# Kernel optimization log

Measured on AMD Instinct MI355X. Metric: run time of the kernel, lower is better.

The kernel has to match this reference:

```python
import jax, jax.numpy as jnp
import numpy as np

MAX_LENGTH = 256
WIDTH = 4


def _attention_matrix(a, b):
    # a, b: (B, M, D) with M = max_length + width - 1
    # euclidean match score: 1 / (1 + ||a_i - b_j||_2)
    sq = (
        jnp.sum(a * a, axis=-1)[:, :, None]
        + jnp.sum(b * b, axis=-1)[:, None, :]
        - 2.0 * jnp.einsum('bid,bjd->bij', a, b)
    )
    dist = jnp.sqrt(jnp.maximum(sq, 0.0))
    return 1.0 / (1.0 + dist)  # (B, M, M)


def reference(x1, x2):
    # x1, x2: (B, 1, M, D), M = MAX_LENGTH + WIDTH - 1
    a = x1[:, 0]  # (B, M, D)
    b = x2[:, 0]
    A = _attention_matrix(a, b)  # (B, M, M), A[b,i,j] = score(a_i, b_j)
    # row_sum over dim i of A[:,:,k] weights x1 column k; col analogously for x2.
    w_a = jnp.sum(A, axis=1)  # (B, M): sum_i A[i, k]
    w_b = jnp.sum(A, axis=2)  # (B, M): sum_j A[k, j]
    y1 = w_a[:, :, None] * a  # (B, M, D)
    y2 = w_b[:, :, None] * b
    # sliding-window sum of width WIDTH: w[j] = sum_{k=j}^{j+WIDTH-1} y[k]
    w1 = sum(y1[:, d:d + MAX_LENGTH, :] for d in range(WIDTH))
    w2 = sum(y2[:, d:d + MAX_LENGTH, :] for d in range(WIDTH))
    return (w1[:, None], w2[:, None])  # (B, 1, MAX_LENGTH, D) each


def setup_inputs() -> dict:
    key = jax.random.key(0)
    k1, k2 = jax.random.split(key)
    B, M, D = 128, MAX_LENGTH + WIDTH - 1, 512
    x1 = jax.random.normal(k1, (B, 1, M, D), dtype=jnp.float32)
    x2 = jax.random.normal(k2, (B, 1, M, D), dtype=jnp.float32)
    return {"x1": x1, "x2": x2}
```

## Files before the change

kernel.cpp:

```cpp
#include <hip/hip_runtime.h>

#define BATCH 128
#define M 259
#define D 512
#define T 256
#define NM (BATCH * M)
#define OUTHALF (BATCH * T * D)

typedef __bf16 bf16;
typedef __bf16 bf16x4 __attribute__((ext_vector_type(4)));
typedef __bf16 bf16x8 __attribute__((ext_vector_type(8)));
typedef float f32x4 __attribute__((ext_vector_type(4)));


__global__ void k_norms(const float* __restrict__ x1, const float* __restrict__ x2,
                        float* __restrict__ ws) {
    int row  = blockIdx.x * 4 + (threadIdx.x >> 6);
    int lane = threadIdx.x & 63;
    if (row >= NM) return;
    const float4* p1 = (const float4*)(x1 + (size_t)row * D);
    const float4* p2 = (const float4*)(x2 + (size_t)row * D);
    float s1 = 0.f, s2 = 0.f;
#pragma unroll
    for (int q = 0; q < 2; ++q) {
        float4 v = p1[lane + q * 64];
        s1 += v.x * v.x + v.y * v.y + v.z * v.z + v.w * v.w;
        float4 u = p2[lane + q * 64];
        s2 += u.x * u.x + u.y * u.y + u.z * u.z + u.w * u.w;
    }
#pragma unroll
    for (int off = 32; off > 0; off >>= 1) {
        s1 += __shfl_xor(s1, off);
        s2 += __shfl_xor(s2, off);
    }
    if (lane == 0) {
        ws[row]          = s1;
        ws[NM + row]     = s2;
        ws[2 * NM + row] = 0.f;
        ws[3 * NM + row] = 0.f;
    }
}

#define BT 144
#define BK 64

__global__ void k_pairs(const float* __restrict__ x1, const float* __restrict__ x2,
                        float* __restrict__ ws) {
    __shared__ __align__(16) bf16 As[BT * BK];
    __shared__ __align__(16) bf16 Bs[BT * BK];

    int s   = blockIdx.x;
    int bid = (s & 7) * 64 + (s >> 3);
    int b   = bid >> 2;
    int ti  = (bid >> 1) & 1;
    int tj  = bid & 1;
    int i0  = ti * BT, j0 = tj * BT;

    int t    = threadIdx.x;
    int lane = t & 63;
    int w    = t / 64;
    int wm   = w / 3, wn = w % 3;
    int iw   = i0 + wm * 48;
    int jw   = j0 + wn * 48;

    const float* Ab = x1 + (size_t)b * M * D;
    const float* Bb = x2 + (size_t)b * M * D;

    const float* pa[4];
    const float* pb[4];
    int c4 = (t & 15) * 4;
#pragma unroll
    for (int p = 0; p < 4; ++p) {
        int row = p * 36 + (t >> 4);
        int ra = min(i0 + row, M - 1);
        int rb = min(j0 + row, M - 1);
        pa[p] = Ab + (size_t)ra * D + c4;
        pb[p] = Bb + (size_t)rb * D + c4;
    }
    int wslot   = (t & 15) >> 1;
    int wwithin = (t & 1) * 4;
    int wr_off[4];
#pragma unroll
    for (int p = 0; p < 4; ++p) {
        int row = p * 36 + (t >> 4);
        wr_off[p] = row * BK + ((wslot ^ (row & 7)) << 3) + wwithin;
    }

    int a_off[3][2], b_off[3][2];
#pragma unroll
    for (int fm = 0; fm < 3; ++fm) {
        int rowa = wm * 48 + fm * 16 + (lane & 15);
        int rowb = wn * 48 + fm * 16 + (lane & 15);
#pragma unroll
        for (int kk = 0; kk < 2; ++kk) {
            int slot = kk * 4 + (lane >> 4);
            a_off[fm][kk] = rowa * BK + ((slot ^ (rowa & 7)) << 3);
            b_off[fm][kk] = rowb * BK + ((slot ^ (rowb & 7)) << 3);
        }
    }

    f32x4 acc[3][3];
#pragma unroll
    for (int fm = 0; fm < 3; ++fm)
#pragma unroll
        for (int fn = 0; fn < 3; ++fn) acc[fm][fn] = (f32x4)0.f;

    for (int k0 = 0; k0 < D; k0 += BK) {
        float4 va[4], vb[4];
#pragma unroll
        for (int p = 0; p < 4; ++p) {
            va[p] = *(const float4*)(pa[p] + k0);
            vb[p] = *(const float4*)(pb[p] + k0);
        }
        __syncthreads();
#pragma unroll
        for (int p = 0; p < 4; ++p) {
            *(bf16x4*)&As[wr_off[p]] = bf16x4{ (bf16)va[p].x, (bf16)va[p].y, (bf16)va[p].z, (bf16)va[p].w };
            *(bf16x4*)&Bs[wr_off[p]] = bf16x4{ (bf16)vb[p].x, (bf16)vb[p].y, (bf16)vb[p].z, (bf16)vb[p].w };
        }
        __syncthreads();
#pragma unroll
        for (int kk = 0; kk < 2; ++kk) {
            bf16x8 af[3], bfr[3];
#pragma unroll
            for (int fm = 0; fm < 3; ++fm) af[fm]  = *(const bf16x8*)&As[a_off[fm][kk]];
#pragma unroll
            for (int fn = 0; fn < 3; ++fn) bfr[fn] = *(const bf16x8*)&Bs[b_off[fn][kk]];
#pragma unroll
            for (int fm = 0; fm < 3; ++fm)
#pragma unroll
                for (int fn = 0; fn < 3; ++fn)
                    acc[fm][fn] = __builtin_amdgcn_mfma_f32_16x16x32_bf16(
                        af[fm], bfr[fn], acc[fm][fn], 0, 0, 0);
        }
    }

    int b_off_w = b * M;
    float na_[3][4], nb_[3];
#pragma unroll
    for (int fm = 0; fm < 3; ++fm)
#pragma unroll
        for (int r = 0; r < 4; ++r) {
            int i = iw + fm * 16 + (lane >> 4) * 4 + r;
            na_[fm][r] = (i < M) ? ws[b_off_w + i] : 0.f;
        }
#pragma unroll
    for (int fn = 0; fn < 3; ++fn) {
        int j = jw + fn * 16 + (lane & 15);
        nb_[fn] = (j < M) ? ws[NM + b_off_w + j] : 0.f;
    }

    float rs[3][4], cs[3];
#pragma unroll
    for (int fm = 0; fm < 3; ++fm)
#pragma unroll
        for (int r = 0; r < 4; ++r) rs[fm][r] = 0.f;
#pragma unroll
    for (int fn = 0; fn < 3; ++fn) cs[fn] = 0.f;

#pragma unroll
    for (int fm = 0; fm < 3; ++fm) {
#pragma unroll
        for (int fn = 0; fn < 3; ++fn) {
#pragma unroll
            for (int r = 0; r < 4; ++r) {
                int i = iw + fm * 16 + (lane >> 4) * 4 + r;
                int j = jw + fn * 16 + (lane & 15);
                float av = 0.f;
                if (i < M && j < M) {
                    float sq   = na_[fm][r] + nb_[fn] - 2.f * acc[fm][fn][r];
                    float dist = sqrtf(fmaxf(sq, 0.f));
                    av = 1.f / (1.f + dist);
                }
                rs[fm][r] += av;
                cs[fn]    += av;
            }
        }
    }

#pragma unroll
    for (int fm = 0; fm < 3; ++fm)
#pragma unroll
        for (int r = 0; r < 4; ++r) {
            float v = rs[fm][r];
            v += __shfl_xor(v, 1); v += __shfl_xor(v, 2);
            v += __shfl_xor(v, 4); v += __shfl_xor(v, 8);
            int i = iw + fm * 16 + (lane >> 4) * 4 + r;
            if ((lane & 15) == 0 && i < M) atomicAdd(&ws[3 * NM + b_off_w + i], v);
        }
#pragma unroll
    for (int fn = 0; fn < 3; ++fn) {
        float v = cs[fn];
        v += __shfl_xor(v, 16); v += __shfl_xor(v, 32);
        int j = jw + fn * 16 + (lane & 15);
        if ((lane >> 4) == 0 && j < M) atomicAdd(&ws[2 * NM + b_off_w + j], v);
    }
}

__global__ void k_out(const float* __restrict__ x1, const float* __restrict__ x2,
                      const float* __restrict__ ws, float* __restrict__ out) {
    int bid   = blockIdx.x;
    int which = bid & 1;
    int tc    = (bid >> 1) & 7;
    int b     = bid >> 4;
    int d4    = threadIdx.x << 2;
    const float* src  = which ? x2 : x1;
    const float* wgt  = ws + (which ? 3 * NM : 2 * NM) + b * M;
    const float* rows = src + (size_t)b * M * D + d4;
    float* o = out + (size_t)which * OUTHALF + ((size_t)b * T + tc * 32) * D + d4;
    int t0 = tc * 32;
    float4 v0 = *(const float4*)(rows + (size_t)(t0 + 0) * D);
    float4 v1 = *(const float4*)(rows + (size_t)(t0 + 1) * D);
    float4 v2 = *(const float4*)(rows + (size_t)(t0 + 2) * D);
    float s0 = wgt[t0 + 0], s1 = wgt[t0 + 1], s2 = wgt[t0 + 2];
#pragma unroll 4
    for (int tt = 0; tt < 32; ++tt) {
        float4 v3 = *(const float4*)(rows + (size_t)(t0 + tt + 3) * D);
        float s3  = wgt[t0 + tt + 3];
        float4 r;
        r.x = s0 * v0.x + s1 * v1.x + s2 * v2.x + s3 * v3.x;
        r.y = s0 * v0.y + s1 * v1.y + s2 * v2.y + s3 * v3.y;
        r.z = s0 * v0.z + s1 * v1.z + s2 * v2.z + s3 * v3.z;
        r.w = s0 * v0.w + s1 * v1.w + s2 * v2.w + s3 * v3.w;
        *(float4*)(o + (size_t)tt * D) = r;
        v0 = v1; v1 = v2; v2 = v3;
        s0 = s1; s1 = s2; s2 = s3;
    }
}

extern "C" void kernel_launch(void* const* d_in, const int* in_sizes, int n_in,
                              void* d_out, int out_size, void* d_ws, size_t ws_size,
                              hipStream_t stream) {
    const float* x1 = (const float*)d_in[0];
    const float* x2 = (const float*)d_in[1];
    float* out = (float*)d_out;
    float* ws  = (float*)d_ws;

    k_norms<<<NM / 4, 256, 0, stream>>>(x1, x2, ws);
    k_pairs<<<512, 576, 0, stream>>>(x1, x2, ws);
    k_out<<<BATCH * 16, 128, 0, stream>>>(x1, x2, ws, out);
}
```

Baseline: 119.3 us.

## Replace shared-memory 144x144 tiles with single-wave 64x64 register-direct MFMA tiles

The pairwise kernel drops its LDS-staged 144x144 tiles (9 waves per block, 512 blocks). It now launches 3200 single-wave blocks, each covering a 64x64 tile and loading bf16 MFMA operands straight from global memory into registers, with no shared memory or barriers. This removes the sync and LDS traffic and gives more blocks for latency hiding. In exchange each fp32 row is re-read by 5 tiles, which raises L2 traffic and the number of uncoalesced strided loads.

Result: slower. 174.5 us (+46.3%).

```diff
diff --git a/kernel.cpp b/kernel.cpp
--- a/kernel.cpp
+++ b/kernel.cpp
@@ -8,7 +8,6 @@
 #define OUTHALF (BATCH * T * D)
 
 typedef __bf16 bf16;
-typedef __bf16 bf16x4 __attribute__((ext_vector_type(4)));
 typedef __bf16 bf16x8 __attribute__((ext_vector_type(8)));
 typedef float f32x4 __attribute__((ext_vector_type(4)));
 
@@ -41,159 +40,120 @@
     }
 }
 
-#define BT 144
-#define BK 64
-
+#define NT5 5
+
+__launch_bounds__(64)
 __global__ void k_pairs(const float* __restrict__ x1, const float* __restrict__ x2,
                         float* __restrict__ ws) {
-    __shared__ __align__(16) bf16 As[BT * BK];
-    __shared__ __align__(16) bf16 Bs[BT * BK];
-
     int s   = blockIdx.x;
-    int bid = (s & 7) * 64 + (s >> 3);
-    int b   = bid >> 2;
-    int ti  = (bid >> 1) & 1;
-    int tj  = bid & 1;
-    int i0  = ti * BT, j0 = tj * BT;
-
-    int t    = threadIdx.x;
-    int lane = t & 63;
-    int w    = t / 64;
-    int wm   = w / 3, wn = w % 3;
-    int iw   = i0 + wm * 48;
-    int jw   = j0 + wn * 48;
+    int bid = (s & 7) * 400 + (s >> 3);
+    int b   = bid / 25;
+    int tt  = bid % 25;
+    int ti  = tt / 5, tj = tt % 5;
+    int i0  = ti * 64, j0 = tj * 64;
+
+    int lane = threadIdx.x;
+    int r16  = lane & 15;
+    int ks4  = lane >> 4;
 
     const float* Ab = x1 + (size_t)b * M * D;
     const float* Bb = x2 + (size_t)b * M * D;
 
-    const float* pa[4];
-    const float* pb[4];
-    int c4 = (t & 15) * 4;
-#pragma unroll
-    for (int p = 0; p < 4; ++p) {
-        int row = p * 36 + (t >> 4);
-        int ra = min(i0 + row, M - 1);
-        int rb = min(j0 + row, M - 1);
-        pa[p] = Ab + (size_t)ra * D + c4;
-        pb[p] = Bb + (size_t)rb * D + c4;
-    }
-    int wslot   = (t & 15) >> 1;
-    int wwithin = (t & 1) * 4;
-    int wr_off[4];
-#pragma unroll
-    for (int p = 0; p < 4; ++p) {
-        int row = p * 36 + (t >> 4);
-        wr_off[p] = row * BK + ((wslot ^ (row & 7)) << 3) + wwithin;
-    }
-
-    int a_off[3][2], b_off[3][2];
-#pragma unroll
-    for (int fm = 0; fm < 3; ++fm) {
-        int rowa = wm * 48 + fm * 16 + (lane & 15);
-        int rowb = wn * 48 + fm * 16 + (lane & 15);
-#pragma unroll
-        for (int kk = 0; kk < 2; ++kk) {
-            int slot = kk * 4 + (lane >> 4);
-            a_off[fm][kk] = rowa * BK + ((slot ^ (rowa & 7)) << 3);
-            b_off[fm][kk] = rowb * BK + ((slot ^ (rowb & 7)) << 3);
-        }
-    }
-
-    f32x4 acc[3][3];
-#pragma unroll
-    for (int fm = 0; fm < 3; ++fm)
-#pragma unroll
-        for (int fn = 0; fn < 3; ++fn) acc[fm][fn] = (f32x4)0.f;
-
-    for (int k0 = 0; k0 < D; k0 += BK) {
-        float4 va[4], vb[4];
-#pragma unroll
-        for (int p = 0; p < 4; ++p) {
-            va[p] = *(const float4*)(pa[p] + k0);
-            vb[p] = *(const float4*)(pb[p] + k0);
-        }
-        __syncthreads();
-#pragma unroll
-        for (int p = 0; p < 4; ++p) {
-            *(bf16x4*)&As[wr_off[p]] = bf16x4{ (bf16)va[p].x, (bf16)va[p].y, (bf16)va[p].z, (bf16)va[p].w };
-            *(bf16x4*)&Bs[wr_off[p]] = bf16x4{ (bf16)vb[p].x, (bf16)vb[p].y, (bf16)vb[p].z, (bf16)vb[p].w };
-        }
-        __syncthreads();
-#pragma unroll
-        for (int kk = 0; kk < 2; ++kk) {
-            bf16x8 af[3], bfr[3];
-#pragma unroll
-            for (int fm = 0; fm < 3; ++fm) af[fm]  = *(const bf16x8*)&As[a_off[fm][kk]];
-#pragma unroll
-            for (int fn = 0; fn < 3; ++fn) bfr[fn] = *(const bf16x8*)&Bs[b_off[fn][kk]];
-#pragma unroll
-            for (int fm = 0; fm < 3; ++fm)
-#pragma unroll
-                for (int fn = 0; fn < 3; ++fn)
-                    acc[fm][fn] = __builtin_amdgcn_mfma_f32_16x16x32_bf16(
-                        af[fm], bfr[fn], acc[fm][fn], 0, 0, 0);
-        }
+    const float* pA[4];
+    const float* pB[4];
+#pragma unroll
+    for (int f = 0; f < 4; ++f) {
+        int ra = min(i0 + f * 16 + r16, M - 1);
+        int rb = min(j0 + f * 16 + r16, M - 1);
+        pA[f] = Ab + (size_t)ra * D + ks4 * 8;
+        pB[f] = Bb + (size_t)rb * D + ks4 * 8;
+    }
+
+    f32x4 acc[4][4];
+#pragma unroll
+    for (int fi = 0; fi < 4; ++fi)
+#pragma unroll
+        for (int fj = 0; fj < 4; ++fj) acc[fi][fj] = (f32x4)0.f;
+
+    for (int ks = 0; ks < 16; ++ks) {
+        int k0 = ks * 32;
+        bf16x8 af[4], bfv[4];
+#pragma unroll
+        for (int f = 0; f < 4; ++f) {
+            float4 lo = *(const float4*)(pA[f] + k0);
+            float4 hi = *(const float4*)(pA[f] + k0 + 4);
+            af[f] = bf16x8{ (bf16)lo.x, (bf16)lo.y, (bf16)lo.z, (bf16)lo.w,
+                            (bf16)hi.x, (bf16)hi.y, (bf16)hi.z, (bf16)hi.w };
+            float4 lo2 = *(const float4*)(pB[f] + k0);
+            float4 hi2 = *(const float4*)(pB[f] + k0 + 4);
+            bfv[f] = bf16x8{ (bf16)lo2.x, (bf16)lo2.y, (bf16)lo2.z, (bf16)lo2.w,
+                             (bf16)hi2.x, (bf16)hi2.y, (bf16)hi2.z, (bf16)hi2.w };
+        }
+#pragma unroll
+        for (int fi = 0; fi < 4; ++fi)
+#pragma unroll
+            for (int fj = 0; fj < 4; ++fj)
+                acc[fi][fj] = __builtin_amdgcn_mfma_f32_16x16x32_bf16(
+                    af[fi], bfv[fj], acc[fi][fj], 0, 0, 0);
     }
 
     int b_off_w = b * M;
-    float na_[3][4], nb_[3];
-#pragma unroll
-    for (int fm = 0; fm < 3; ++fm)
+    float na_[4][4], nb_[4];
+#pragma unroll
+    for (int f = 0; f < 4; ++f) {
 #pragma unroll
         for (int r = 0; r < 4; ++r) {
-            int i = iw + fm * 16 + (lane >> 4) * 4 + r;
-            na_[fm][r] = (i < M) ? ws[b_off_w + i] : 0.f;
-        }
-#pragma unroll
-    for (int fn = 0; fn < 3; ++fn) {
-        int j = jw + fn * 16 + (lane & 15);
-        nb_[fn] = (j < M) ? ws[NM + b_off_w + j] : 0.f;
-    }
-
-    float rs[3][4], cs[3];
-#pragma unroll
-    for (int fm = 0; fm < 3; ++fm)
-#pragma unroll
-        for (int r = 0; r < 4; ++r) rs[fm][r] = 0.f;
-#pragma unroll
-    for (int fn = 0; fn < 3; ++fn) cs[fn] = 0.f;
-
-#pragma unroll
-    for (int fm = 0; fm < 3; ++fm) {
-#pragma unroll
-        for (int fn = 0; fn < 3; ++fn) {
+            int i = i0 + f * 16 + ks4 * 4 + r;
+            na_[f][r] = (i < M) ? ws[b_off_w + i] : 0.f;
+        }
+        int j = j0 + f * 16 + r16;
+        nb_[f] = (j < M) ? ws[NM + b_off_w + j] : 0.f;
+    }
+
+    float rs[4][4], cs[4];
+#pragma unroll
+    for (int f = 0; f < 4; ++f) {
+#pragma unroll
+        for (int r = 0; r < 4; ++r) rs[f][r] = 0.f;
+        cs[f] = 0.f;
+    }
+
+#pragma unroll
+    for (int fi = 0; fi < 4; ++fi) {
+#pragma unroll
+        for (int fj = 0; fj < 4; ++fj) {
 #pragma unroll
             for (int r = 0; r < 4; ++r) {
-                int i = iw + fm * 16 + (lane >> 4) * 4 + r;
-                int j = jw + fn * 16 + (lane & 15);
+                int i = i0 + fi * 16 + ks4 * 4 + r;
+                int j = j0 + fj * 16 + r16;
                 float av = 0.f;
                 if (i < M && j < M) {
-                    float sq   = na_[fm][r] + nb_[fn] - 2.f * acc[fm][fn][r];
+                    float sq   = na_[fi][r] + nb_[fj] - 2.f * acc[fi][fj][r];
                     float dist = sqrtf(fmaxf(sq, 0.f));
                     av = 1.f / (1.f + dist);
                 }
-                rs[fm][r] += av;
-                cs[fn]    += av;
+                rs[fi][r] += av;
+                cs[fj]    += av;
             }
         }
     }
 
 #pragma unroll
-    for (int fm = 0; fm < 3; ++fm)
+    for (int f = 0; f < 4; ++f)
 #pragma unroll
         for (int r = 0; r < 4; ++r) {
-            float v = rs[fm][r];
+            float v = rs[f][r];
             v += __shfl_xor(v, 1); v += __shfl_xor(v, 2);
             v += __shfl_xor(v, 4); v += __shfl_xor(v, 8);
-            int i = iw + fm * 16 + (lane >> 4) * 4 + r;
-            if ((lane & 15) == 0 && i < M) atomicAdd(&ws[3 * NM + b_off_w + i], v);
-        }
-#pragma unroll
-    for (int fn = 0; fn < 3; ++fn) {
-        float v = cs[fn];
+            int i = i0 + f * 16 + ks4 * 4 + r;
+            if (r16 == 0 && i < M) atomicAdd(&ws[3 * NM + b_off_w + i], v);
+        }
+#pragma unroll
+    for (int f = 0; f < 4; ++f) {
+        float v = cs[f];
         v += __shfl_xor(v, 16); v += __shfl_xor(v, 32);
-        int j = jw + fn * 16 + (lane & 15);
-        if ((lane >> 4) == 0 && j < M) atomicAdd(&ws[2 * NM + b_off_w + j], v);
+        int j = j0 + f * 16 + r16;
+        if (ks4 == 0 && j < M) atomicAdd(&ws[2 * NM + b_off_w + j], v);
     }
 }
 
@@ -237,6 +197,6 @@
     float* ws  = (float*)d_ws;
 
     k_norms<<<NM / 4, 256, 0, stream>>>(x1, x2, ws);
-    k_pairs<<<512, 576, 0, stream>>>(x1, x2, ws);
+    k_pairs<<<BATCH * 25, 64, 0, stream>>>(x1, x2, ws);
     k_out<<<BATCH * 16, 128, 0, stream>>>(x1, x2, ws, out);
 }
```
